# Kernel tuning notes

Hardware: AMD Instinct MI355X
Metric: run time of the kernel (lower is better)

Reference implementation:

```python
import jax, jax.numpy as jnp
import numpy as np

N_HOST, N_FLOW, E = 20000, 200000, 600000
D_IN, D_H, D_OUT = 64, 128, 32
NEG_SLOPE = 0.01  # F.leaky_relu default


def setup_inputs() -> dict:
    key = jax.random.key(0)
    ks = jax.random.split(key, 20)

    def w(k, shape):
        # kaiming-uniform-ish init scale (matches Linear fan-in scaling)
        lim = 1.0 / np.sqrt(shape[0])
        return jax.random.uniform(k, shape, jnp.float32, -lim, lim)

    return {
        "x_host": jax.random.normal(ks[0], (N_HOST, D_IN), jnp.float32),
        "x_flow": jax.random.normal(ks[1], (N_FLOW, D_IN), jnp.float32),
        "src_hf": jax.random.randint(ks[2], (E,), 0, N_HOST, dtype=jnp.int32),
        "dst_hf": jax.random.randint(ks[3], (E,), 0, N_FLOW, dtype=jnp.int32),
        "src_fh": jax.random.randint(ks[4], (E,), 0, N_FLOW, dtype=jnp.int32),
        "dst_fh": jax.random.randint(ks[5], (E,), 0, N_HOST, dtype=jnp.int32),
        "W0_hf_l": w(ks[6], (D_IN, D_H)), "W0_hf_r": w(ks[7], (D_IN, D_H)),
        "b0_hf": jnp.zeros((D_H,), jnp.float32),
        "W0_fh_l": w(ks[8], (D_IN, D_H)), "W0_fh_r": w(ks[9], (D_IN, D_H)),
        "b0_fh": jnp.zeros((D_H,), jnp.float32),
        "W1_hf_l": w(ks[10], (D_H, D_H)), "W1_hf_r": w(ks[11], (D_H, D_H)),
        "b1_hf": jnp.zeros((D_H,), jnp.float32),
        "W1_fh_l": w(ks[12], (D_H, D_H)), "W1_fh_r": w(ks[13], (D_H, D_H)),
        "b1_fh": jnp.zeros((D_H,), jnp.float32),
        "W_out": w(ks[14], (D_H, D_OUT)),
        "b_out": jnp.zeros((D_OUT,), jnp.float32),
    }


def _seg_mean(x, src, dst, n_dst):
    """Mean-aggregate src-node features over edges into n_dst segments."""
    s = jax.ops.segment_sum(x[src], dst, num_segments=n_dst)      # [n_dst, d]
    cnt = jax.ops.segment_sum(jnp.ones(src.shape, x.dtype), dst, num_segments=n_dst)
    return s / jnp.clip(cnt, 1.0)[:, None]


def _sage(x_src, x_dst, src, dst, Wl, Wr, b, n_dst):
    # SAGEConv: lin_l(mean_agg) + bias + lin_r(x_dst)
    agg = _seg_mean(x_src, src, dst, n_dst)
    return agg @ Wl + b + x_dst @ Wr


def reference(x_host, x_flow, src_hf, dst_hf, src_fh, dst_fh,
              W0_hf_l, W0_hf_r, b0_hf, W0_fh_l, W0_fh_r, b0_fh,
              W1_hf_l, W1_hf_r, b1_hf, W1_fh_l, W1_fh_r, b1_fh,
              W_out, b_out):
    lrelu = lambda v: jnp.where(v > 0, v, NEG_SLOPE * v)

    # layer 0
    h_flow = lrelu(_sage(x_host, x_flow, src_hf, dst_hf, W0_hf_l, W0_hf_r, b0_hf, N_FLOW))
    h_host = lrelu(_sage(x_flow, x_host, src_fh, dst_fh, W0_fh_l, W0_fh_r, b0_fh, N_HOST))

    # layer 1
    g_flow = lrelu(_sage(h_host, h_flow, src_hf, dst_hf, W1_hf_l, W1_hf_r, b1_hf, N_FLOW))
    g_host = lrelu(_sage(h_flow, h_host, src_fh, dst_fh, W1_fh_l, W1_fh_r, b1_fh, N_HOST))
    del g_host  # computed (matches module) but only 'flow' feeds the head

    return g_flow @ W_out + b_out  # [N_FLOW, D_OUT]
```

## Files before the change

kernel.cpp:

```cpp
#include <hip/hip_runtime.h>


#define N_HOST 20000
#define N_FLOW 200000
#define NEDGE  600000
#define D_IN   64
#define D_H    128
#define D_OUT  32
#define NSEG   (N_FLOW + N_HOST)
#define NBKT_F 196
#define NBKT_H 79
#define NBKT   (NBKT_F + NBKT_H)
#define NEB    586

typedef unsigned short u16;
typedef unsigned int   u32;
typedef short bf16x8 __attribute__((ext_vector_type(8)));
typedef float f32x4  __attribute__((ext_vector_type(4)));

__device__ __forceinline__ float bfh(u16 h) { return __uint_as_float(((u32)h) << 16); }
__device__ __forceinline__ u16 fbh(float f) {
    u32 u = __float_as_uint(f);
    return (u16)((u + 0x7fffu + ((u >> 16) & 1u)) >> 16);
}
__device__ __forceinline__ u32 packbf(float x, float y) {
    return (u32)fbh(x) | ((u32)fbh(y) << 16);
}

__global__ void k_prep(const float* __restrict__ W0_hf_l, const float* __restrict__ W0_hf_r,
                       const float* __restrict__ W0_fh_l, const float* __restrict__ W0_fh_r,
                       const float* __restrict__ W1_l, const float* __restrict__ W1_r,
                       const float* __restrict__ Wout,
                       u16* __restrict__ WT0_hf, u16* __restrict__ WT0_fh,
                       u16* __restrict__ WT1_l, u16* __restrict__ WT1_r,
                       u16* __restrict__ WTo) {
    int b = blockIdx.x, t = threadIdx.x;
    u16 tmp[8];
    if (b < 32) {
        int e = (b & 7) * 2048 + t * 8;
        int n = e >> 7, k0 = e & 127;
        if (b < 8) {
#pragma unroll
            for (int j = 0; j < 8; j++) {
                int k = k0 + j;
                tmp[j] = fbh(k < 64 ? W0_hf_l[k * D_H + n] : W0_hf_r[(k - 64) * D_H + n]);
            }
            *(uint4*)(WT0_hf + n * 128 + k0) = *(uint4*)tmp;
        } else if (b < 16) {
#pragma unroll
            for (int j = 0; j < 8; j++) {
                int k = k0 + j;
                tmp[j] = fbh(k < 64 ? W0_fh_l[k * D_H + n] : W0_fh_r[(k - 64) * D_H + n]);
            }
            *(uint4*)(WT0_fh + n * 128 + k0) = *(uint4*)tmp;
        } else if (b < 24) {
#pragma unroll
            for (int j = 0; j < 8; j++) tmp[j] = fbh(W1_l[(k0 + j) * D_H + n]);
            *(uint4*)(WT1_l + n * 128 + k0) = *(uint4*)tmp;
        } else {
#pragma unroll
            for (int j = 0; j < 8; j++) tmp[j] = fbh(W1_r[(k0 + j) * D_H + n]);
            *(uint4*)(WT1_r + n * 128 + k0) = *(uint4*)tmp;
        }
    } else {
        int e = (b - 32) * 2048 + t * 8;
        int n = e >> 7, k0 = e & 127;
#pragma unroll
        for (int j = 0; j < 8; j++) tmp[j] = fbh(Wout[(k0 + j) * D_OUT + n]);
        *(uint4*)(WTo + n * 128 + k0) = *(uint4*)tmp;
    }
}

__device__ __forceinline__ int bucket_of(int combined_node) {
    return (combined_node < N_FLOW) ? (combined_node >> 10)
                                    : (NBKT_F + ((combined_node - N_FLOW) >> 8));
}

__global__ void kb1(const int* __restrict__ dst_hf, const int* __restrict__ dst_fh,
                    int* __restrict__ bcnt) {
    __shared__ int h[NBKT];
    int t = threadIdx.x;
    for (int j = t; j < NBKT; j += 256) h[j] = 0;
    __syncthreads();
    int base = blockIdx.x * 2048;
#pragma unroll
    for (int i = 0; i < 8; i++) {
        int e = base + t + i * 256;
        if (e < 2 * NEDGE) {
            int bkt = (e < NEDGE) ? (dst_hf[e] >> 10)
                                  : (NBKT_F + (dst_fh[e - NEDGE] >> 8));
            atomicAdd(&h[bkt], 1);
        }
    }
    __syncthreads();
    for (int j = t; j < NBKT; j += 256)
        if (h[j]) atomicAdd(&bcnt[j], h[j]);
}

__global__ void scanB(const int* __restrict__ bcnt, int* __restrict__ ebase) {
    __shared__ int sp[512];
    int t = threadIdx.x;
    int v = (t < NBKT) ? bcnt[t] : 0;
    sp[t] = v;
    __syncthreads();
    for (int d = 1; d < 512; d <<= 1) {
        int x = (t >= d) ? sp[t - d] : 0;
        __syncthreads();
        sp[t] += x;
        __syncthreads();
    }
    if (t < NBKT) ebase[t] = sp[t] - v;
    if (t == NBKT - 1) ebase[NBKT] = sp[t];
}

__global__ void kb2(const int* __restrict__ src_hf, const int* __restrict__ dst_hf,
                    const int* __restrict__ src_fh, const int* __restrict__ dst_fh,
                    const int* __restrict__ ebase, int* __restrict__ bcur,
                    int2* __restrict__ binE) {
    __shared__ int lh[NBKT];
    __shared__ int lb[NBKT];
    int t = threadIdx.x;
    for (int j = t; j < NBKT; j += 256) lh[j] = 0;
    __syncthreads();
    int base = blockIdx.x * 2048;
    int mybkt[8], myrank[8], mysrc[8], mydst[8];
#pragma unroll
    for (int i = 0; i < 8; i++) {
        int e = base + t + i * 256;
        mybkt[i] = -1;
        if (e < 2 * NEDGE) {
            int s, d;
            if (e < NEDGE) { s = src_hf[e]; d = dst_hf[e]; }
            else           { s = src_fh[e - NEDGE]; d = dst_fh[e - NEDGE] + N_FLOW; }
            int bkt = bucket_of(d);
            mybkt[i] = bkt; mysrc[i] = s; mydst[i] = d;
            myrank[i] = atomicAdd(&lh[bkt], 1);
        }
    }
    __syncthreads();
    for (int j = t; j < NBKT; j += 256)
        lb[j] = lh[j] ? atomicAdd(&bcur[j], lh[j]) : 0;
    __syncthreads();
#pragma unroll
    for (int i = 0; i < 8; i++) {
        if (mybkt[i] >= 0) {
            int pos = ebase[mybkt[i]] + lb[mybkt[i]] + myrank[i];
            binE[pos] = make_int2(mysrc[i], mydst[i]);
        }
    }
}

__global__ __launch_bounds__(256) void kb3(const int2* __restrict__ binE,
                                           const int* __restrict__ ebase,
                                           int* __restrict__ off, int* __restrict__ csr) {
    __shared__ int deg[1024];
    __shared__ int ts[256];
    int b = blockIdx.x, t = threadIdx.x;
    int nbase, ncnt;
    if (b < NBKT_F) { nbase = b << 10; ncnt = min(1024, N_FLOW - nbase); }
    else { nbase = N_FLOW + ((b - NBKT_F) << 8); ncnt = min(256, NSEG - nbase); }
    int e0 = ebase[b], e1 = ebase[b + 1];
    for (int i = t; i < 1024; i += 256) deg[i] = 0;
    __syncthreads();
    for (int e = e0 + t; e < e1; e += 256) {
        int2 p = binE[e];
        atomicAdd(&deg[p.y - nbase], 1);
    }
    __syncthreads();
    int loc[4]; int s = 0;
#pragma unroll
    for (int j = 0; j < 4; j++) { loc[j] = s; s += deg[t * 4 + j]; }
    ts[t] = s;
    __syncthreads();
    for (int d = 1; d < 256; d <<= 1) {
        int x = (t >= d) ? ts[t - d] : 0;
        __syncthreads();
        ts[t] += x;
        __syncthreads();
    }
    int base2 = e0 + ts[t] - s;
    int dsave[4];
#pragma unroll
    for (int j = 0; j < 4; j++) dsave[j] = deg[t * 4 + j];
    __syncthreads();
#pragma unroll
    for (int j = 0; j < 4; j++) {
        int idx = t * 4 + j;
        int st = base2 + loc[j];
        deg[idx] = st;
        if (idx < ncnt) off[nbase + idx] = st + dsave[j];
    }
    __syncthreads();
    for (int e = e0 + t; e < e1; e += 256) {
        int2 p = binE[e];
        int r = atomicAdd(&deg[p.y - nbase], 1);
        csr[r] = p.x;
    }
}

__global__ void k_agg0(const float* __restrict__ x_host, const float* __restrict__ x_flow,
                       const int* __restrict__ off, const int* __restrict__ csr,
                       u16* __restrict__ agg0f, u16* __restrict__ agg0h) {
    int t = blockIdx.x * 256 + threadIdx.x;
    int n = t >> 4;
    int c = (t & 15) << 2;
    if (n >= NSEG) return;
    int start = (n == 0) ? 0 : off[n - 1];
    int end = off[n];
    float4 acc = make_float4(0.f, 0.f, 0.f, 0.f);
    const float* xs = (n < N_FLOW) ? x_host : x_flow;
    for (int e = start; e < end; e++) {
        int s = csr[e];
        float4 v = *(const float4*)(xs + s * D_IN + c);
        acc.x += v.x; acc.y += v.y; acc.z += v.z; acc.w += v.w;
    }
    float inv = (end > start) ? 1.f / (float)(end - start) : 0.f;
    uint2 o;
    o.x = packbf(acc.x * inv, acc.y * inv);
    o.y = packbf(acc.z * inv, acc.w * inv);
    if (n < N_FLOW) *(uint2*)(agg0f + n * D_IN + c) = o;
    else            *(uint2*)(agg0h + (n - N_FLOW) * D_IN + c) = o;
}

__global__ void k_agg1(const u16* __restrict__ hT, const int* __restrict__ off,
                       const int* __restrict__ csr, u16* __restrict__ agg1m) {
    int t = blockIdx.x * 256 + threadIdx.x;
    int n = t >> 4;
    int c = (t & 15) << 3;
    if (n >= N_FLOW) return;
    int start = (n == 0) ? 0 : off[n - 1];
    int end = off[n];
    float acc[8] = {0.f, 0.f, 0.f, 0.f, 0.f, 0.f, 0.f, 0.f};
    for (int e = start; e < end; e++) {
        int s = csr[e];
        uint4 u = *(const uint4*)(hT + s * D_H + c);
        acc[0] += __uint_as_float(u.x << 16);
        acc[1] += __uint_as_float(u.x & 0xffff0000u);
        acc[2] += __uint_as_float(u.y << 16);
        acc[3] += __uint_as_float(u.y & 0xffff0000u);
        acc[4] += __uint_as_float(u.z << 16);
        acc[5] += __uint_as_float(u.z & 0xffff0000u);
        acc[6] += __uint_as_float(u.w << 16);
        acc[7] += __uint_as_float(u.w & 0xffff0000u);
    }
    float inv = (end > start) ? 1.f / (float)(end - start) : 0.f;
    uint4 o;
    o.x = packbf(acc[0] * inv, acc[1] * inv);
    o.y = packbf(acc[2] * inv, acc[3] * inv);
    o.z = packbf(acc[4] * inv, acc[5] * inv);
    o.w = packbf(acc[6] * inv, acc[7] * inv);
    *(uint4*)(agg1m + n * D_H + c) = o;
}

template <bool DUAL, bool RELU>
__global__ __launch_bounds__(256) void k_mfma(
    const u16* __restrict__ A1, const float* __restrict__ A2,
    const u16* __restrict__ WT, const float* __restrict__ bias,
    u16* __restrict__ OUT, int M) {
    __shared__ __align__(16) u16 sA[64 * 136];
    __shared__ __align__(16) u16 sW[128 * 136];
    const int t = threadIdx.x;
    const int m0 = blockIdx.x * 64;
#pragma unroll
    for (int i = 0; i < 8; i++) {
        int q = t + i * 256;
        int row = q >> 4, seg = q & 15;
        *(uint4*)(&sW[row * 136 + seg * 8]) = *(const uint4*)(WT + row * 128 + seg * 8);
    }
#pragma unroll
    for (int i = 0; i < 4; i++) {
        int q = t + i * 256;
        int r = q >> 4, seg = q & 15;
        int row = m0 + r;
        uint4 val = make_uint4(0u, 0u, 0u, 0u);
        if (row < M) {
            if (DUAL) {
                if (seg < 8) {
                    val = *(const uint4*)(A1 + row * 64 + seg * 8);
                } else {
                    float4 f0 = *(const float4*)(A2 + row * 64 + (seg - 8) * 8);
                    float4 f1 = *(const float4*)(A2 + row * 64 + (seg - 8) * 8 + 4);
                    val.x = packbf(f0.x, f0.y); val.y = packbf(f0.z, f0.w);
                    val.z = packbf(f1.x, f1.y); val.w = packbf(f1.z, f1.w);
                }
            } else {
                val = *(const uint4*)(A1 + row * 128 + seg * 8);
            }
        }
        *(uint4*)(&sA[r * 136 + seg * 8]) = val;
    }
    __syncthreads();
    const int w = t >> 6, ln = t & 63, l15 = ln & 15, quad = ln >> 4;
    const u16* pA = sA + (w * 16 + l15) * 136 + quad * 8;
    const u16* pB = sW + l15 * 136 + quad * 8;
    f32x4 acc[8];
#pragma unroll
    for (int tt = 0; tt < 8; tt++) acc[tt] = (f32x4){0.f, 0.f, 0.f, 0.f};
#pragma unroll
    for (int s = 0; s < 4; s++) {
        bf16x8 a = *(const bf16x8*)(pA + s * 32);
#pragma unroll
        for (int tt = 0; tt < 8; tt++) {
            bf16x8 b = *(const bf16x8*)(pB + tt * 2176 + s * 32);
            acc[tt] = __builtin_amdgcn_mfma_f32_16x16x32_bf16(a, b, acc[tt], 0, 0, 0);
        }
    }
#pragma unroll
    for (int tt = 0; tt < 8; tt++) {
        int col = tt * 16 + l15;
        float bv = bias ? bias[col] : 0.f;
#pragma unroll
        for (int i = 0; i < 4; i++) {
            int row = m0 + w * 16 + quad * 4 + i;
            if (row < M) {
                float v = acc[tt][i] + bv;
                if (RELU) v = v > 0.f ? v : 0.01f * v;
                OUT[row * D_H + col] = fbh(v);
            }
        }
    }
}

__global__ __launch_bounds__(256) void k_final(
    const u16* __restrict__ A, const u16* __restrict__ WT1r,
    const float* __restrict__ b1, const u16* __restrict__ aggm,
    const u16* __restrict__ WTo, const float* __restrict__ bout,
    float* __restrict__ OUT, int M) {
    __shared__ __align__(16) u16 sA[64 * 136];
    __shared__ __align__(16) u16 sW[128 * 136];
    const int t = threadIdx.x;
    const int m0 = blockIdx.x * 64;
#pragma unroll
    for (int i = 0; i < 8; i++) {
        int q = t + i * 256;
        int row = q >> 4, seg = q & 15;
        *(uint4*)(&sW[row * 136 + seg * 8]) = *(const uint4*)(WT1r + row * 128 + seg * 8);
    }
#pragma unroll
    for (int i = 0; i < 4; i++) {
        int q = t + i * 256;
        int r = q >> 4, seg = q & 15;
        int row = m0 + r;
        uint4 val = make_uint4(0u, 0u, 0u, 0u);
        if (row < M) val = *(const uint4*)(A + row * D_H + seg * 8);
        *(uint4*)(&sA[r * 136 + seg * 8]) = val;
    }
    __syncthreads();
    const int w = t >> 6, ln = t & 63, l15 = ln & 15, quad = ln >> 4;
    bf16x8 bo[2][4];
#pragma unroll
    for (int tt = 0; tt < 2; tt++)
#pragma unroll
        for (int s = 0; s < 4; s++)
            bo[tt][s] = *(const bf16x8*)(WTo + (tt * 16 + l15) * 128 + s * 32 + quad * 8);
    const u16* pA = sA + (w * 16 + l15) * 136 + quad * 8;
    const u16* pB = sW + l15 * 136 + quad * 8;
    f32x4 acc[8];
#pragma unroll
    for (int tt = 0; tt < 8; tt++) acc[tt] = (f32x4){0.f, 0.f, 0.f, 0.f};
#pragma unroll
    for (int s = 0; s < 4; s++) {
        bf16x8 a = *(const bf16x8*)(pA + s * 32);
#pragma unroll
        for (int tt = 0; tt < 8; tt++) {
            bf16x8 b = *(const bf16x8*)(pB + tt * 2176 + s * 32);
            acc[tt] = __builtin_amdgcn_mfma_f32_16x16x32_bf16(a, b, acc[tt], 0, 0, 0);
        }
    }
#pragma unroll
    for (int tt = 0; tt < 8; tt++) {
        int col = tt * 16 + l15;
        float bv = b1[col];
#pragma unroll
        for (int i = 0; i < 4; i++) {
            int rl = w * 16 + quad * 4 + i;
            int row = m0 + rl;
            float ag = (row < M) ? bfh(aggm[row * D_H + col]) : 0.f;
            float v = acc[tt][i] + ag + bv;
            v = v > 0.f ? v : 0.01f * v;
            sA[rl * 136 + col] = fbh(v);
        }
    }
    f32x4 acc2[2];
    acc2[0] = (f32x4){0.f, 0.f, 0.f, 0.f};
    acc2[1] = (f32x4){0.f, 0.f, 0.f, 0.f};
#pragma unroll
    for (int s = 0; s < 4; s++) {
        bf16x8 g = *(const bf16x8*)(pA + s * 32);
        acc2[0] = __builtin_amdgcn_mfma_f32_16x16x32_bf16(g, bo[0][s], acc2[0], 0, 0, 0);
        acc2[1] = __builtin_amdgcn_mfma_f32_16x16x32_bf16(g, bo[1][s], acc2[1], 0, 0, 0);
    }
#pragma unroll
    for (int tt = 0; tt < 2; tt++) {
        int col = tt * 16 + l15;
        float bv = bout[col];
#pragma unroll
        for (int i = 0; i < 4; i++) {
            int row = m0 + w * 16 + quad * 4 + i;
            if (row < M) OUT[row * D_OUT + col] = acc2[tt][i] + bv;
        }
    }
}

extern "C" void kernel_launch(void* const* d_in, const int* in_sizes, int n_in,
                              void* d_out, int out_size, void* d_ws, size_t ws_size,
                              hipStream_t stream) {
    const float* x_host  = (const float*)d_in[0];
    const float* x_flow  = (const float*)d_in[1];
    const int* src_hf  = (const int*)d_in[2];
    const int* dst_hf  = (const int*)d_in[3];
    const int* src_fh  = (const int*)d_in[4];
    const int* dst_fh  = (const int*)d_in[5];
    const float* W0_hf_l = (const float*)d_in[6];
    const float* W0_hf_r = (const float*)d_in[7];
    const float* b0_hf   = (const float*)d_in[8];
    const float* W0_fh_l = (const float*)d_in[9];
    const float* W0_fh_r = (const float*)d_in[10];
    const float* b0_fh   = (const float*)d_in[11];
    const float* W1_hf_l = (const float*)d_in[12];
    const float* W1_hf_r = (const float*)d_in[13];
    const float* b1_hf   = (const float*)d_in[14];
    const float* W_out   = (const float*)d_in[18];
    const float* b_out   = (const float*)d_in[19];
    float* out = (float*)d_out;

    char* ws = (char*)d_ws;
    int* off    = (int*)(ws + 0);
    int* csr    = (int*)(ws + 880000);
    u16* h_flow = (u16*)(ws + 5680000);
    u16* hT     = (u16*)(ws + 56880000);
    u16* agg1m  = (u16*)(ws + 62000000);
    int2* binE  = (int2*)(ws + 62000000);
    u16* agg0f  = (u16*)(ws + 62000000);
    u16* agg0h  = (u16*)(ws + 87600000);
    u16* h_host = (u16*)(ws + 90160000);
    int* bcnt   = (int*)(ws + 113200000);
    int* bcur   = (int*)(ws + 113201280);
    int* ebase  = (int*)(ws + 113202560);
    u16* WT0_hf = (u16*)(ws + 114080000);
    u16* WT0_fh = (u16*)(ws + 114112768);
    u16* WT1_l  = (u16*)(ws + 114145536);
    u16* WT1_r  = (u16*)(ws + 114178304);
    u16* WTo    = (u16*)(ws + 114211072);

    hipMemsetAsync(bcnt, 0, 2560, stream);
    k_prep<<<34, 256, 0, stream>>>(W0_hf_l, W0_hf_r, W0_fh_l, W0_fh_r, W1_hf_l, W1_hf_r,
                                   W_out, WT0_hf, WT0_fh, WT1_l, WT1_r, WTo);
    kb1<<<NEB, 256, 0, stream>>>(dst_hf, dst_fh, bcnt);
    scanB<<<1, 512, 0, stream>>>(bcnt, ebase);
    kb2<<<NEB, 256, 0, stream>>>(src_hf, dst_hf, src_fh, dst_fh, ebase, bcur, binE);
    kb3<<<NBKT, 256, 0, stream>>>(binE, ebase, off, csr);
    k_agg0<<<(NSEG * 16 + 255) / 256, 256, 0, stream>>>(x_host, x_flow, off, csr, agg0f, agg0h);
    k_mfma<true, true><<<3125, 256, 0, stream>>>(agg0f, x_flow, WT0_hf, b0_hf, h_flow, N_FLOW);
    k_mfma<true, true><<<313, 256, 0, stream>>>(agg0h, x_host, WT0_fh, b0_fh, h_host, N_HOST);
    k_mfma<false, false><<<313, 256, 0, stream>>>(h_host, nullptr, WT1_l, nullptr, hT, N_HOST);
    k_agg1<<<(N_FLOW * 16 + 255) / 256, 256, 0, stream>>>(hT, off, csr, agg1m);
    k_final<<<3125, 256, 0, stream>>>(h_flow, WT1_r, b1_hf, agg1m, WTo, b_out, out, N_FLOW);
}
```

Before: 415.6 us.

## Fuse mean aggregation into SAGE GEMM kernels and pre-convert inputs to bf16

Removes the standalone aggregation kernels. The neighbour mean is now computed inside the MFMA kernels that consume it: k_sage for layer 0, and k_final for the layer-1 flow aggregation, which writes into reused shared memory. A new k_cvt kernel converts x_flow and x_host to bf16 once, so gathers read half the bytes. This also removes the agg0/agg1 intermediate writes and reads. The cost is less gather parallelism per node (8 or 16 threads per row inside the GEMM block), possible latency stalls in the GEMM kernels, and an extra pass to convert the inputs.

```diff
diff --git a/kernel.cpp b/kernel.cpp
--- a/kernel.cpp
+++ b/kernel.cpp
@@ -71,6 +71,23 @@
     }
 }
 
+__global__ void k_cvt(const float* __restrict__ xf, const float* __restrict__ xh,
+                      u16* __restrict__ xfb, u16* __restrict__ xhb) {
+    int t = blockIdx.x * 256 + threadIdx.x;
+    const int TF = (N_FLOW * D_IN) / 8;
+    const int TT = TF + (N_HOST * D_IN) / 8;
+    if (t >= TT) return;
+    const float* src; u16* dst; int base;
+    if (t < TF) { src = xf; dst = xfb; base = t * 8; }
+    else        { src = xh; dst = xhb; base = (t - TF) * 8; }
+    float4 f0 = *(const float4*)(src + base);
+    float4 f1 = *(const float4*)(src + base + 4);
+    uint4 o;
+    o.x = packbf(f0.x, f0.y); o.y = packbf(f0.z, f0.w);
+    o.z = packbf(f1.x, f1.y); o.w = packbf(f1.z, f1.w);
+    *(uint4*)(dst + base) = o;
+}
+
 __device__ __forceinline__ int bucket_of(int combined_node) {
     return (combined_node < N_FLOW) ? (combined_node >> 10)
                                     : (NBKT_F + ((combined_node - N_FLOW) >> 8));
@@ -198,63 +215,9 @@
     }
 }
 
-__global__ void k_agg0(const float* __restrict__ x_host, const float* __restrict__ x_flow,
-                       const int* __restrict__ off, const int* __restrict__ csr,
-                       u16* __restrict__ agg0f, u16* __restrict__ agg0h) {
-    int t = blockIdx.x * 256 + threadIdx.x;
-    int n = t >> 4;
-    int c = (t & 15) << 2;
-    if (n >= NSEG) return;
-    int start = (n == 0) ? 0 : off[n - 1];
-    int end = off[n];
-    float4 acc = make_float4(0.f, 0.f, 0.f, 0.f);
-    const float* xs = (n < N_FLOW) ? x_host : x_flow;
-    for (int e = start; e < end; e++) {
-        int s = csr[e];
-        float4 v = *(const float4*)(xs + s * D_IN + c);
-        acc.x += v.x; acc.y += v.y; acc.z += v.z; acc.w += v.w;
-    }
-    float inv = (end > start) ? 1.f / (float)(end - start) : 0.f;
-    uint2 o;
-    o.x = packbf(acc.x * inv, acc.y * inv);
-    o.y = packbf(acc.z * inv, acc.w * inv);
-    if (n < N_FLOW) *(uint2*)(agg0f + n * D_IN + c) = o;
-    else            *(uint2*)(agg0h + (n - N_FLOW) * D_IN + c) = o;
-}
-
-__global__ void k_agg1(const u16* __restrict__ hT, const int* __restrict__ off,
-                       const int* __restrict__ csr, u16* __restrict__ agg1m) {
-    int t = blockIdx.x * 256 + threadIdx.x;
-    int n = t >> 4;
-    int c = (t & 15) << 3;
-    if (n >= N_FLOW) return;
-    int start = (n == 0) ? 0 : off[n - 1];
-    int end = off[n];
-    float acc[8] = {0.f, 0.f, 0.f, 0.f, 0.f, 0.f, 0.f, 0.f};
-    for (int e = start; e < end; e++) {
-        int s = csr[e];
-        uint4 u = *(const uint4*)(hT + s * D_H + c);
-        acc[0] += __uint_as_float(u.x << 16);
-        acc[1] += __uint_as_float(u.x & 0xffff0000u);
-        acc[2] += __uint_as_float(u.y << 16);
-        acc[3] += __uint_as_float(u.y & 0xffff0000u);
-        acc[4] += __uint_as_float(u.z << 16);
-        acc[5] += __uint_as_float(u.z & 0xffff0000u);
-        acc[6] += __uint_as_float(u.w << 16);
-        acc[7] += __uint_as_float(u.w & 0xffff0000u);
-    }
-    float inv = (end > start) ? 1.f / (float)(end - start) : 0.f;
-    uint4 o;
-    o.x = packbf(acc[0] * inv, acc[1] * inv);
-    o.y = packbf(acc[2] * inv, acc[3] * inv);
-    o.z = packbf(acc[4] * inv, acc[5] * inv);
-    o.w = packbf(acc[6] * inv, acc[7] * inv);
-    *(uint4*)(agg1m + n * D_H + c) = o;
-}
-
-template <bool DUAL, bool RELU>
-__global__ __launch_bounds__(256) void k_mfma(
-    const u16* __restrict__ A1, const float* __restrict__ A2,
+__global__ __launch_bounds__(256) void k_sage(
+    const u16* __restrict__ gpool, const u16* __restrict__ dpool,
+    const int* __restrict__ off, const int* __restrict__ csr, int segbase,
     const u16* __restrict__ WT, const float* __restrict__ bias,
     u16* __restrict__ OUT, int M) {
     __shared__ __align__(16) u16 sA[64 * 136];
@@ -268,26 +231,44 @@
         *(uint4*)(&sW[row * 136 + seg * 8]) = *(const uint4*)(WT + row * 128 + seg * 8);
     }
 #pragma unroll
-    for (int i = 0; i < 4; i++) {
-        int q = t + i * 256;
-        int r = q >> 4, seg = q & 15;
+    for (int i = 0; i < 2; i++) {
+        int q = t + i * 256;
+        int r = q >> 3, c = q & 7;
         int row = m0 + r;
-        uint4 val = make_uint4(0u, 0u, 0u, 0u);
+        uint4 v = make_uint4(0u, 0u, 0u, 0u);
+        if (row < M) v = *(const uint4*)(dpool + row * 64 + c * 8);
+        *(uint4*)(&sA[r * 136 + 64 + c * 8]) = v;
+    }
+#pragma unroll
+    for (int i = 0; i < 2; i++) {
+        int q = t + i * 256;
+        int r = q >> 3, c = q & 7;
+        int row = m0 + r;
+        uint4 o = make_uint4(0u, 0u, 0u, 0u);
         if (row < M) {
-            if (DUAL) {
-                if (seg < 8) {
-                    val = *(const uint4*)(A1 + row * 64 + seg * 8);
-                } else {
-                    float4 f0 = *(const float4*)(A2 + row * 64 + (seg - 8) * 8);
-                    float4 f1 = *(const float4*)(A2 + row * 64 + (seg - 8) * 8 + 4);
-                    val.x = packbf(f0.x, f0.y); val.y = packbf(f0.z, f0.w);
-                    val.z = packbf(f1.x, f1.y); val.w = packbf(f1.z, f1.w);
-                }
-            } else {
-                val = *(const uint4*)(A1 + row * 128 + seg * 8);
+            int idx = segbase + row;
+            int st = (idx == 0) ? 0 : off[idx - 1];
+            int en = off[idx];
+            float a[8] = {0.f, 0.f, 0.f, 0.f, 0.f, 0.f, 0.f, 0.f};
+            for (int e = st; e < en; e++) {
+                int s = csr[e];
+                uint4 u = *(const uint4*)(gpool + s * 64 + c * 8);
+                a[0] += __uint_as_float(u.x << 16);
+                a[1] += __uint_as_float(u.x & 0xffff0000u);
+                a[2] += __uint_as_float(u.y << 16);
+                a[3] += __uint_as_float(u.y & 0xffff0000u);
+                a[4] += __uint_as_float(u.z << 16);
+                a[5] += __uint_as_float(u.z & 0xffff0000u);
+                a[6] += __uint_as_float(u.w << 16);
+                a[7] += __uint_as_float(u.w & 0xffff0000u);
             }
-        }
-        *(uint4*)(&sA[r * 136 + seg * 8]) = val;
+            float inv = (en > st) ? 1.f / (float)(en - st) : 0.f;
+            o.x = packbf(a[0] * inv, a[1] * inv);
+            o.y = packbf(a[2] * inv, a[3] * inv);
+            o.z = packbf(a[4] * inv, a[5] * inv);
+            o.w = packbf(a[6] * inv, a[7] * inv);
+        }
+        *(uint4*)(&sA[r * 136 + c * 8]) = o;
     }
     __syncthreads();
     const int w = t >> 6, ln = t & 63, l15 = ln & 15, quad = ln >> 4;
@@ -308,26 +289,77 @@
 #pragma unroll
     for (int tt = 0; tt < 8; tt++) {
         int col = tt * 16 + l15;
-        float bv = bias ? bias[col] : 0.f;
+        float bv = bias[col];
 #pragma unroll
         for (int i = 0; i < 4; i++) {
             int row = m0 + w * 16 + quad * 4 + i;
             if (row < M) {
                 float v = acc[tt][i] + bv;
-                if (RELU) v = v > 0.f ? v : 0.01f * v;
+                v = v > 0.f ? v : 0.01f * v;
                 OUT[row * D_H + col] = fbh(v);
             }
         }
     }
 }
 
+__global__ __launch_bounds__(256) void k_mfma(
+    const u16* __restrict__ A, const u16* __restrict__ WT,
+    u16* __restrict__ OUT, int M) {
+    __shared__ __align__(16) u16 sA[64 * 136];
+    __shared__ __align__(16) u16 sW[128 * 136];
+    const int t = threadIdx.x;
+    const int m0 = blockIdx.x * 64;
+#pragma unroll
+    for (int i = 0; i < 8; i++) {
+        int q = t + i * 256;
+        int row = q >> 4, seg = q & 15;
+        *(uint4*)(&sW[row * 136 + seg * 8]) = *(const uint4*)(WT + row * 128 + seg * 8);
+    }
+#pragma unroll
+    for (int i = 0; i < 4; i++) {
+        int q = t + i * 256;
+        int r = q >> 4, seg = q & 15;
+        int row = m0 + r;
+        uint4 val = make_uint4(0u, 0u, 0u, 0u);
+        if (row < M) val = *(const uint4*)(A + row * 128 + seg * 8);
+        *(uint4*)(&sA[r * 136 + seg * 8]) = val;
+    }
+    __syncthreads();
+    const int w = t >> 6, ln = t & 63, l15 = ln & 15, quad = ln >> 4;
+    const u16* pA = sA + (w * 16 + l15) * 136 + quad * 8;
+    const u16* pB = sW + l15 * 136 + quad * 8;
+    f32x4 acc[8];
+#pragma unroll
+    for (int tt = 0; tt < 8; tt++) acc[tt] = (f32x4){0.f, 0.f, 0.f, 0.f};
+#pragma unroll
+    for (int s = 0; s < 4; s++) {
+        bf16x8 a = *(const bf16x8*)(pA + s * 32);
+#pragma unroll
+        for (int tt = 0; tt < 8; tt++) {
+            bf16x8 b = *(const bf16x8*)(pB + tt * 2176 + s * 32);
+            acc[tt] = __builtin_amdgcn_mfma_f32_16x16x32_bf16(a, b, acc[tt], 0, 0, 0);
+        }
+    }
+#pragma unroll
+    for (int tt = 0; tt < 8; tt++) {
+        int col = tt * 16 + l15;
+#pragma unroll
+        for (int i = 0; i < 4; i++) {
+            int row = m0 + w * 16 + quad * 4 + i;
+            if (row < M) OUT[row * D_H + col] = fbh(acc[tt][i]);
+        }
+    }
+}
+
 __global__ __launch_bounds__(256) void k_final(
     const u16* __restrict__ A, const u16* __restrict__ WT1r,
-    const float* __restrict__ b1, const u16* __restrict__ aggm,
+    const float* __restrict__ b1, const u16* __restrict__ hT,
+    const int* __restrict__ off, const int* __restrict__ csr,
     const u16* __restrict__ WTo, const float* __restrict__ bout,
     float* __restrict__ OUT, int M) {
     __shared__ __align__(16) u16 sA[64 * 136];
     __shared__ __align__(16) u16 sW[128 * 136];
+    u16* sAg = sW;
     const int t = threadIdx.x;
     const int m0 = blockIdx.x * 64;
 #pragma unroll
@@ -367,6 +399,38 @@
             acc[tt] = __builtin_amdgcn_mfma_f32_16x16x32_bf16(a, b, acc[tt], 0, 0, 0);
         }
     }
+    __syncthreads();
+#pragma unroll
+    for (int i = 0; i < 4; i++) {
+        int q = t + i * 256;
+        int r = q >> 4, c = q & 15;
+        int row = m0 + r;
+        uint4 o = make_uint4(0u, 0u, 0u, 0u);
+        if (row < M) {
+            int st = (row == 0) ? 0 : off[row - 1];
+            int en = off[row];
+            float a[8] = {0.f, 0.f, 0.f, 0.f, 0.f, 0.f, 0.f, 0.f};
+            for (int e = st; e < en; e++) {
+                int s = csr[e];
+                uint4 u = *(const uint4*)(hT + s * D_H + c * 8);
+                a[0] += __uint_as_float(u.x << 16);
+                a[1] += __uint_as_float(u.x & 0xffff0000u);
+                a[2] += __uint_as_float(u.y << 16);
+                a[3] += __uint_as_float(u.y & 0xffff0000u);
+                a[4] += __uint_as_float(u.z << 16);
+                a[5] += __uint_as_float(u.z & 0xffff0000u);
+                a[6] += __uint_as_float(u.w << 16);
+                a[7] += __uint_as_float(u.w & 0xffff0000u);
+            }
+            float inv = (en > st) ? 1.f / (float)(en - st) : 0.f;
+            o.x = packbf(a[0] * inv, a[1] * inv);
+            o.y = packbf(a[2] * inv, a[3] * inv);
+            o.z = packbf(a[4] * inv, a[5] * inv);
+            o.w = packbf(a[6] * inv, a[7] * inv);
+        }
+        *(uint4*)(&sAg[r * 136 + c * 8]) = o;
+    }
+    __syncthreads();
 #pragma unroll
     for (int tt = 0; tt < 8; tt++) {
         int col = tt * 16 + l15;
@@ -374,8 +438,7 @@
 #pragma unroll
         for (int i = 0; i < 4; i++) {
             int rl = w * 16 + quad * 4 + i;
-            int row = m0 + rl;
-            float ag = (row < M) ? bfh(aggm[row * D_H + col]) : 0.f;
+            float ag = bfh(sAg[rl * 136 + col]);
             float v = acc[tt][i] + ag + bv;
             v = v > 0.f ? v : 0.01f * v;
             sA[rl * 136 + col] = fbh(v);
@@ -425,35 +488,33 @@
     float* out = (float*)d_out;
 
     char* ws = (char*)d_ws;
-    int* off    = (int*)(ws + 0);
-    int* csr    = (int*)(ws + 880000);
-    u16* h_flow = (u16*)(ws + 5680000);
-    u16* hT     = (u16*)(ws + 56880000);
-    u16* agg1m  = (u16*)(ws + 62000000);
-    int2* binE  = (int2*)(ws + 62000000);
-    u16* agg0f  = (u16*)(ws + 62000000);
-    u16* agg0h  = (u16*)(ws + 87600000);
-    u16* h_host = (u16*)(ws + 90160000);
-    int* bcnt   = (int*)(ws + 113200000);
-    int* bcur   = (int*)(ws + 113201280);
-    int* ebase  = (int*)(ws + 113202560);
-    u16* WT0_hf = (u16*)(ws + 114080000);
-    u16* WT0_fh = (u16*)(ws + 114112768);
-    u16* WT1_l  = (u16*)(ws + 114145536);
-    u16* WT1_r  = (u16*)(ws + 114178304);
-    u16* WTo    = (u16*)(ws + 114211072);
+    int*  off    = (int*)(ws + 0);
+    int*  csr    = (int*)(ws + 880000);
+    u16*  h_flow = (u16*)(ws + 5680000);
+    u16*  hT     = (u16*)(ws + 56880000);
+    u16*  h_host = (u16*)(ws + 62000000);
+    u16*  xfb    = (u16*)(ws + 67120000);
+    u16*  xhb    = (u16*)(ws + 92720000);
+    int2* binE   = (int2*)(ws + 95280000);
+    int*  bcnt   = (int*)(ws + 104880000);
+    int*  bcur   = (int*)(ws + 104881280);
+    int*  ebase  = (int*)(ws + 104882560);
+    u16*  WT0_hf = (u16*)(ws + 104883840);
+    u16*  WT0_fh = (u16*)(ws + 104916608);
+    u16*  WT1_l  = (u16*)(ws + 104949376);
+    u16*  WT1_r  = (u16*)(ws + 104982144);
+    u16*  WTo    = (u16*)(ws + 105014912);
 
     hipMemsetAsync(bcnt, 0, 2560, stream);
     k_prep<<<34, 256, 0, stream>>>(W0_hf_l, W0_hf_r, W0_fh_l, W0_fh_r, W1_hf_l, W1_hf_r,
                                    W_out, WT0_hf, WT0_fh, WT1_l, WT1_r, WTo);
+    k_cvt<<<6875, 256, 0, stream>>>(x_flow, x_host, xfb, xhb);
     kb1<<<NEB, 256, 0, stream>>>(dst_hf, dst_fh, bcnt);
     scanB<<<1, 512, 0, stream>>>(bcnt, ebase);
     kb2<<<NEB, 256, 0, stream>>>(src_hf, dst_hf, src_fh, dst_fh, ebase, bcur, binE);
     kb3<<<NBKT, 256, 0, stream>>>(binE, ebase, off, csr);
-    k_agg0<<<(NSEG * 16 + 255) / 256, 256, 0, stream>>>(x_host, x_flow, off, csr, agg0f, agg0h);
-    k_mfma<true, true><<<3125, 256, 0, stream>>>(agg0f, x_flow, WT0_hf, b0_hf, h_flow, N_FLOW);
-    k_mfma<true, true><<<313, 256, 0, stream>>>(agg0h, x_host, WT0_fh, b0_fh, h_host, N_HOST);
-    k_mfma<false, false><<<313, 256, 0, stream>>>(h_host, nullptr, WT1_l, nullptr, hT, N_HOST);
-    k_agg1<<<(N_FLOW * 16 + 255) / 256, 256, 0, stream>>>(hT, off, csr, agg1m);
-    k_final<<<3125, 256, 0, stream>>>(h_flow, WT1_r, b1_hf, agg1m, WTo, b_out, out, N_FLOW);
-}
+    k_sage<<<3125, 256, 0, stream>>>(xhb, xfb, off, csr, 0,      WT0_hf, b0_hf, h_flow, N_FLOW);
+    k_sage<<<313, 256, 0, stream>>>(xfb, xhb, off, csr, N_FLOW, WT0_fh, b0_fh, h_host, N_HOST);
+    k_mfma<<<313, 256, 0, stream>>>(h_host, WT1_l, hT, N_HOST);
+    k_final<<<3125, 256, 0, stream>>>(h_flow, WT1_r, b1_hf, hT, off, csr, WTo, b_out, out, N_FLOW);
+}
```

Measured after the change: 436.2 us. 1.05x slower.
